# Kernel optimization log

Hardware: AMD Instinct MI355X
Metric: run time of the kernel (lower is better)

The kernel has to match this reference:

```python
import jax, jax.numpy as jnp
import numpy as np

N_NODES = 100000
N_EDGES = 3200000
FEAT = 64  # pos(32) + vel(32)
OUT_DIM = 2


def setup_inputs() -> dict:
    key = jax.random.key(0)
    k1, k2, k3, k4, k5, k6, k7, k8 = jax.random.split(key, 8)
    pos = jax.random.normal(k1, (N_NODES, 32), dtype=jnp.float32)
    vel = jax.random.normal(k2, (N_NODES, 32), dtype=jnp.float32)
    edge_index = jax.random.randint(k3, (2, N_EDGES), 0, N_NODES, dtype=jnp.int64 if jax.config.jax_enable_x64 else jnp.int32)
    s = 1.0 / np.sqrt(FEAT)
    W_rel = jax.random.uniform(k4, (FEAT, FEAT), jnp.float32, -s, s)
    b_rel = jax.random.uniform(k5, (FEAT,), jnp.float32, -s, s)
    W_root = jax.random.uniform(k6, (FEAT, FEAT), jnp.float32, -s, s)
    W_pred = jax.random.uniform(k7, (FEAT, OUT_DIM), jnp.float32, -s, s)
    b_pred = jax.random.uniform(k8, (OUT_DIM,), jnp.float32, -s, s)
    return {"pos": pos, "vel": vel, "edge_index": edge_index,
            "W_rel": W_rel, "b_rel": b_rel, "W_root": W_root,
            "W_pred": W_pred, "b_pred": b_pred}


def reference(pos, vel, edge_index, W_rel, b_rel, W_root, W_pred, b_pred):
    # h = cat([pos, vel], -1)  -> [N, 64]
    h = jnp.concatenate([pos, vel], axis=-1)
    src, dst = edge_index[0], edge_index[1]
    # GraphConv (PyG, aggr='add'): out_i = lin_rel(sum_{j->i} h_j) + lin_root(h_i)
    msgs = h[src]  # [E, 64] irregular gather
    agg = jax.ops.segment_sum(msgs, dst, num_segments=N_NODES)  # [N, 64]
    conv_out = agg @ W_rel + b_rel + h @ W_root
    # lin_pred
    return conv_out @ W_pred + b_pred
```

## Files before the change

### kernel.cpp

```cpp
#include <hip/hip_runtime.h>

#define N_NODES 100000
#define N_EDGES 3200000
#define FEAT 64
#define OUT_DIM 2

#define K_DST 98
#define DST_SZ 1024
#define NPART 8
#define PART_SZ 12500
#define NSUB (K_DST * NPART)
#define CAP_SUB 4468
#define NB 400
#define EPB (N_EDGES / NB)
#define BT 1024


__global__ __launch_bounds__(256) void node_kernel(const float* __restrict__ pos,
                                                   const float* __restrict__ vel,
                                                   const float* __restrict__ W_rel,
                                                   const float* __restrict__ b_rel,
                                                   const float* __restrict__ W_root,
                                                   const float* __restrict__ W_pred,
                                                   const float* __restrict__ b_pred,
                                                   unsigned* __restrict__ y,
                                                   float* __restrict__ out,
                                                   int* __restrict__ gcount) {
    __shared__ float sM[258];
    int t = threadIdx.x;

    if (blockIdx.x == 0)
        for (int i = t; i < NSUB; i += 256) gcount[i] = 0;

    {
        const float* W = (t < 128) ? W_rel : W_root;
        int k = (t & 127) >> 1, o = t & 1;
        float acc = 0.f;
        #pragma unroll
        for (int f = 0; f < FEAT; ++f) acc += W[k * FEAT + f] * W_pred[f * OUT_DIM + o];
        sM[t] = acc;
        if (t < OUT_DIM) {
            float b = b_pred[t];
            #pragma unroll
            for (int f = 0; f < FEAT; ++f) b += b_rel[f] * W_pred[f * OUT_DIM + t];
            sM[256 + t] = b;
        }
    }
    __syncthreads();

    int n = blockIdx.x * 256 + t;
    if (n >= N_NODES) return;

    const float4* p4 = (const float4*)(pos + (size_t)n * 32);
    const float4* v4 = (const float4*)(vel + (size_t)n * 32);
    float h[FEAT];
    #pragma unroll
    for (int i = 0; i < 8; ++i) {
        float4 a = p4[i];
        h[i * 4 + 0] = a.x; h[i * 4 + 1] = a.y; h[i * 4 + 2] = a.z; h[i * 4 + 3] = a.w;
    }
    #pragma unroll
    for (int i = 0; i < 8; ++i) {
        float4 a = v4[i];
        h[32 + i * 4 + 0] = a.x; h[32 + i * 4 + 1] = a.y; h[32 + i * 4 + 2] = a.z; h[32 + i * 4 + 3] = a.w;
    }

    float rel0 = 0.f, rel1 = 0.f, ro0 = 0.f, ro1 = 0.f;
    #pragma unroll
    for (int k = 0; k < FEAT; ++k) {
        float hk = h[k];
        rel0 += hk * sM[2 * k + 0];
        rel1 += hk * sM[2 * k + 1];
        ro0  += hk * sM[128 + 2 * k + 0];
        ro1  += hk * sM[128 + 2 * k + 1];
    }
    unsigned bx = __float_as_uint(rel0);
    unsigned by = __float_as_uint(rel1);
    bx += 0x7FFFu + ((bx >> 16) & 1u);
    by += 0x7FFFu + ((by >> 16) & 1u);
    y[n] = (bx >> 16) | (by & 0xFFFF0000u);
    ((float2*)out)[n] = make_float2(ro0 + sM[256], ro1 + sM[257]);
}

__global__ __launch_bounds__(BT) void binscatter_kernel(const int* __restrict__ edges,
                                                        int* __restrict__ gcount,
                                                        unsigned* __restrict__ scat) {
    __shared__ int hist[NSUB];
    __shared__ int cum[NSUB + 1];
    __shared__ int base[NSUB];
    __shared__ int rpos[NSUB];
    __shared__ unsigned sortbuf[EPB];

    int t = threadIdx.x;
    for (int i = t; i < NSUB; i += BT) hist[i] = 0;
    __syncthreads();

    const int4* s4 = (const int4*)(edges) + blockIdx.x * (EPB / 4);
    const int4* d4 = (const int4*)(edges + N_EDGES) + blockIdx.x * (EPB / 4);
    int4 sreg[2], dreg[2];
    bool valid[2];
    #pragma unroll
    for (int r = 0; r < 2; ++r) {
        int i = t + r * BT;
        valid[r] = (i < EPB / 4);
        if (valid[r]) { sreg[r] = s4[i]; dreg[r] = d4[i]; }
    }

    #pragma unroll
    for (int r = 0; r < 2; ++r) {
        if (!valid[r]) continue;
        int4 s = sreg[r];
        int4 d = dreg[r];
        atomicAdd(&hist[((unsigned)d.x >> 10) * NPART + (unsigned)s.x / PART_SZ], 1);
        atomicAdd(&hist[((unsigned)d.y >> 10) * NPART + (unsigned)s.y / PART_SZ], 1);
        atomicAdd(&hist[((unsigned)d.z >> 10) * NPART + (unsigned)s.z / PART_SZ], 1);
        atomicAdd(&hist[((unsigned)d.w >> 10) * NPART + (unsigned)s.w / PART_SZ], 1);
    }
    __syncthreads();

    for (int i = t; i < NSUB; i += BT) base[i] = atomicAdd(&gcount[i], hist[i]);
    if (t < 64) {
        int lo = t * 13;
        int vals[13];
        int lsum = 0;
        #pragma unroll
        for (int j = 0; j < 13; ++j) {
            int idx = lo + j;
            int v = (idx < NSUB) ? hist[idx] : 0;
            vals[j] = lsum;
            lsum += v;
        }
        int x = lsum;
        #pragma unroll
        for (int d = 1; d < 64; d <<= 1) {
            int up = __shfl_up(x, d);
            if (t >= d) x += up;
        }
        int excl = x - lsum;
        #pragma unroll
        for (int j = 0; j < 13; ++j) {
            int idx = lo + j;
            if (idx < NSUB) { cum[idx] = excl + vals[j]; rpos[idx] = excl + vals[j]; }
        }
        if (t == 63) cum[NSUB] = excl + lsum;
    }
    __syncthreads();

    #pragma unroll
    for (int r = 0; r < 2; ++r) {
        if (!valid[r]) continue;
        int4 s = sreg[r];
        int4 d = dreg[r];
        int k, p;
        k = ((unsigned)d.x >> 10) * NPART + (unsigned)s.x / PART_SZ;
        p = atomicAdd(&rpos[k], 1);
        sortbuf[p] = (unsigned)s.x | (((unsigned)d.x & (DST_SZ - 1)) << 17);
        k = ((unsigned)d.y >> 10) * NPART + (unsigned)s.y / PART_SZ;
        p = atomicAdd(&rpos[k], 1);
        sortbuf[p] = (unsigned)s.y | (((unsigned)d.y & (DST_SZ - 1)) << 17);
        k = ((unsigned)d.z >> 10) * NPART + (unsigned)s.z / PART_SZ;
        p = atomicAdd(&rpos[k], 1);
        sortbuf[p] = (unsigned)s.z | (((unsigned)d.z & (DST_SZ - 1)) << 17);
        k = ((unsigned)d.w >> 10) * NPART + (unsigned)s.w / PART_SZ;
        p = atomicAdd(&rpos[k], 1);
        sortbuf[p] = (unsigned)s.w | (((unsigned)d.w & (DST_SZ - 1)) << 17);
    }
    __syncthreads();

    int wid = t >> 6, lane = t & 63;
    for (int k = wid; k < NSUB; k += BT / 64) {
        int s0 = cum[k], s1 = cum[k + 1], b = base[k];
        for (int j = s0 + lane; j < s1; j += 64) {
            int p = b + (j - s0);
            if (p < CAP_SUB) scat[(size_t)k * CAP_SUB + p] = sortbuf[j];
        }
    }
}

__global__ __launch_bounds__(BT) void accum_partial_kernel(const unsigned* __restrict__ scat,
                                                           const int* __restrict__ gcount,
                                                           const unsigned* __restrict__ y,
                                                           unsigned* __restrict__ partial) {
    __shared__ unsigned yl[PART_SZ];
    __shared__ float accx[DST_SZ];
    __shared__ float accy[DST_SZ];

    int t = threadIdx.x;
    int sub = blockIdx.x;
    int p = sub & (NPART - 1);
    accx[t] = 0.f;
    accy[t] = 0.f;

    const unsigned* yp = y + p * PART_SZ;
    for (int i = t; i < PART_SZ; i += BT) yl[i] = yp[i];
    __syncthreads();

    int c = gcount[sub];
    if (c > CAP_SUB) c = CAP_SUB;
    const unsigned* sl = scat + (size_t)sub * CAP_SUB;
    int pbase = p * PART_SZ;
    for (int i = t; i < c; i += BT) {
        unsigned e = sl[i];
        int slocal = (int)(e & 0x1FFFF) - pbase;
        int dl = e >> 17;
        unsigned v = yl[slocal];
        atomicAdd(&accx[dl], __uint_as_float(v << 16));
        atomicAdd(&accy[dl], __uint_as_float(v & 0xFFFF0000u));
    }
    __syncthreads();

    unsigned bx = __float_as_uint(accx[t]);
    unsigned by = __float_as_uint(accy[t]);
    bx += 0x7FFFu + ((bx >> 16) & 1u);
    by += 0x7FFFu + ((by >> 16) & 1u);
    partial[(size_t)sub * DST_SZ + t] = (bx >> 16) | (by & 0xFFFF0000u);
}

__global__ __launch_bounds__(BT) void merge_kernel(const unsigned* __restrict__ partial,
                                                   float* __restrict__ out) {
    int t = threadIdx.x;
    int kd = blockIdx.x;
    int n = kd * DST_SZ + t;
    if (n >= N_NODES) return;

    float sx = 0.f, sy = 0.f;
    #pragma unroll
    for (int p = 0; p < NPART; ++p) {
        unsigned v = partial[((size_t)kd * NPART + p) * DST_SZ + t];
        sx += __uint_as_float(v << 16);
        sy += __uint_as_float(v & 0xFFFF0000u);
    }
    float2* o2 = (float2*)out;
    float2 cv = o2[n];
    cv.x += sx;
    cv.y += sy;
    o2[n] = cv;
}

extern "C" void kernel_launch(void* const* d_in, const int* in_sizes, int n_in,
                              void* d_out, int out_size, void* d_ws, size_t ws_size,
                              hipStream_t stream) {
    const float* pos    = (const float*)d_in[0];
    const float* vel    = (const float*)d_in[1];
    const int*   edges  = (const int*)d_in[2];
    const float* W_rel  = (const float*)d_in[3];
    const float* b_rel  = (const float*)d_in[4];
    const float* W_root = (const float*)d_in[5];
    const float* W_pred = (const float*)d_in[6];
    const float* b_pred = (const float*)d_in[7];
    float* out = (float*)d_out;

    char* ws = (char*)d_ws;
    unsigned* y       = (unsigned*)(ws + 2048);
    int*      gcount  = (int*)(ws + 402048);
    unsigned* scat    = (unsigned*)(ws + 405184);
    unsigned* partial = (unsigned*)(ws + 14416832);

    int node_blocks = (N_NODES + 255) / 256;
    node_kernel<<<node_blocks, 256, 0, stream>>>(pos, vel, W_rel, b_rel, W_root,
                                                 W_pred, b_pred, y, out, gcount);

    binscatter_kernel<<<NB, BT, 0, stream>>>(edges, gcount, scat);

    accum_partial_kernel<<<NSUB, BT, 0, stream>>>(scat, gcount, y, partial);

    merge_kernel<<<K_DST, BT, 0, stream>>>(partial, out);
}
```

Baseline: 180.8 us.

## Retile destination buckets to 1568 nodes and vectorize partial accumulation loads

The destination bucket size grows from 1024 to 1568 nodes, which cuts the number of sub-buckets from 784 to 512 and raises the per-bucket capacity. The scan is simplified to match. The accumulation kernel now issues all of its global loads up front: node values and edge records are read as uint4 and kept in registers before the shared-memory fill. Each edge chunk is processed in one pass with no loop, and an occupancy hint is added to the launch bounds. This aims to cut block count, per-block overhead and load latency. The cost is a non-power-of-two divide and modulo on destination indices, plus a merge kernel that now computes bucket coordinates per node.

```diff
diff --git a/kernel.cpp b/kernel.cpp
--- a/kernel.cpp
+++ b/kernel.cpp
@@ -5,12 +5,12 @@
 #define FEAT 64
 #define OUT_DIM 2
 
-#define K_DST 98
-#define DST_SZ 1024
+#define K_DST 64
+#define DST_SZ 1568
 #define NPART 8
 #define PART_SZ 12500
 #define NSUB (K_DST * NPART)
-#define CAP_SUB 4468
+#define CAP_SUB 6724
 #define NB 400
 #define EPB (N_EDGES / NB)
 #define BT 1024
@@ -111,25 +111,20 @@
         if (!valid[r]) continue;
         int4 s = sreg[r];
         int4 d = dreg[r];
-        atomicAdd(&hist[((unsigned)d.x >> 10) * NPART + (unsigned)s.x / PART_SZ], 1);
-        atomicAdd(&hist[((unsigned)d.y >> 10) * NPART + (unsigned)s.y / PART_SZ], 1);
-        atomicAdd(&hist[((unsigned)d.z >> 10) * NPART + (unsigned)s.z / PART_SZ], 1);
-        atomicAdd(&hist[((unsigned)d.w >> 10) * NPART + (unsigned)s.w / PART_SZ], 1);
+        atomicAdd(&hist[((unsigned)d.x / DST_SZ) * NPART + (unsigned)s.x / PART_SZ], 1);
+        atomicAdd(&hist[((unsigned)d.y / DST_SZ) * NPART + (unsigned)s.y / PART_SZ], 1);
+        atomicAdd(&hist[((unsigned)d.z / DST_SZ) * NPART + (unsigned)s.z / PART_SZ], 1);
+        atomicAdd(&hist[((unsigned)d.w / DST_SZ) * NPART + (unsigned)s.w / PART_SZ], 1);
     }
     __syncthreads();
 
     for (int i = t; i < NSUB; i += BT) base[i] = atomicAdd(&gcount[i], hist[i]);
     if (t < 64) {
-        int lo = t * 13;
-        int vals[13];
+        int lo = t * 8;
+        int vals[8];
         int lsum = 0;
         #pragma unroll
-        for (int j = 0; j < 13; ++j) {
-            int idx = lo + j;
-            int v = (idx < NSUB) ? hist[idx] : 0;
-            vals[j] = lsum;
-            lsum += v;
-        }
+        for (int j = 0; j < 8; ++j) { int v = hist[lo + j]; vals[j] = lsum; lsum += v; }
         int x = lsum;
         #pragma unroll
         for (int d = 1; d < 64; d <<= 1) {
@@ -138,10 +133,7 @@
         }
         int excl = x - lsum;
         #pragma unroll
-        for (int j = 0; j < 13; ++j) {
-            int idx = lo + j;
-            if (idx < NSUB) { cum[idx] = excl + vals[j]; rpos[idx] = excl + vals[j]; }
-        }
+        for (int j = 0; j < 8; ++j) { cum[lo + j] = excl + vals[j]; rpos[lo + j] = excl + vals[j]; }
         if (t == 63) cum[NSUB] = excl + lsum;
     }
     __syncthreads();
@@ -151,19 +143,19 @@
         if (!valid[r]) continue;
         int4 s = sreg[r];
         int4 d = dreg[r];
-        int k, p;
-        k = ((unsigned)d.x >> 10) * NPART + (unsigned)s.x / PART_SZ;
-        p = atomicAdd(&rpos[k], 1);
-        sortbuf[p] = (unsigned)s.x | (((unsigned)d.x & (DST_SZ - 1)) << 17);
-        k = ((unsigned)d.y >> 10) * NPART + (unsigned)s.y / PART_SZ;
-        p = atomicAdd(&rpos[k], 1);
-        sortbuf[p] = (unsigned)s.y | (((unsigned)d.y & (DST_SZ - 1)) << 17);
-        k = ((unsigned)d.z >> 10) * NPART + (unsigned)s.z / PART_SZ;
-        p = atomicAdd(&rpos[k], 1);
-        sortbuf[p] = (unsigned)s.z | (((unsigned)d.z & (DST_SZ - 1)) << 17);
-        k = ((unsigned)d.w >> 10) * NPART + (unsigned)s.w / PART_SZ;
-        p = atomicAdd(&rpos[k], 1);
-        sortbuf[p] = (unsigned)s.w | (((unsigned)d.w & (DST_SZ - 1)) << 17);
+        int kk, p, dl;
+        kk = (unsigned)d.x / DST_SZ; dl = d.x - kk * DST_SZ;
+        p = atomicAdd(&rpos[kk * NPART + (unsigned)s.x / PART_SZ], 1);
+        sortbuf[p] = (unsigned)s.x | ((unsigned)dl << 17);
+        kk = (unsigned)d.y / DST_SZ; dl = d.y - kk * DST_SZ;
+        p = atomicAdd(&rpos[kk * NPART + (unsigned)s.y / PART_SZ], 1);
+        sortbuf[p] = (unsigned)s.y | ((unsigned)dl << 17);
+        kk = (unsigned)d.z / DST_SZ; dl = d.z - kk * DST_SZ;
+        p = atomicAdd(&rpos[kk * NPART + (unsigned)s.z / PART_SZ], 1);
+        sortbuf[p] = (unsigned)s.z | ((unsigned)dl << 17);
+        kk = (unsigned)d.w / DST_SZ; dl = d.w - kk * DST_SZ;
+        p = atomicAdd(&rpos[kk * NPART + (unsigned)s.w / PART_SZ], 1);
+        sortbuf[p] = (unsigned)s.w | ((unsigned)dl << 17);
     }
     __syncthreads();
 
@@ -177,56 +169,90 @@
     }
 }
 
-__global__ __launch_bounds__(BT) void accum_partial_kernel(const unsigned* __restrict__ scat,
-                                                           const int* __restrict__ gcount,
-                                                           const unsigned* __restrict__ y,
-                                                           unsigned* __restrict__ partial) {
+__global__ __launch_bounds__(BT, 8) void accum_partial_kernel(const unsigned* __restrict__ scat,
+                                                              const int* __restrict__ gcount,
+                                                              const unsigned* __restrict__ y,
+                                                              unsigned* __restrict__ partial) {
     __shared__ unsigned yl[PART_SZ];
     __shared__ float accx[DST_SZ];
     __shared__ float accy[DST_SZ];
 
-    int t = threadIdx.x;
-    int sub = blockIdx.x;
-    int p = sub & (NPART - 1);
-    accx[t] = 0.f;
-    accy[t] = 0.f;
-
-    const unsigned* yp = y + p * PART_SZ;
-    for (int i = t; i < PART_SZ; i += BT) yl[i] = yp[i];
-    __syncthreads();
+    const int t = threadIdx.x;
+    const int sub = blockIdx.x;
+    const int p = sub & (NPART - 1);
 
     int c = gcount[sub];
     if (c > CAP_SUB) c = CAP_SUB;
-    const unsigned* sl = scat + (size_t)sub * CAP_SUB;
-    int pbase = p * PART_SZ;
-    for (int i = t; i < c; i += BT) {
-        unsigned e = sl[i];
-        int slocal = (int)(e & 0x1FFFF) - pbase;
-        int dl = e >> 17;
-        unsigned v = yl[slocal];
-        atomicAdd(&accx[dl], __uint_as_float(v << 16));
-        atomicAdd(&accy[dl], __uint_as_float(v & 0xFFFF0000u));
-    }
-    __syncthreads();
-
-    unsigned bx = __float_as_uint(accx[t]);
-    unsigned by = __float_as_uint(accy[t]);
-    bx += 0x7FFFu + ((bx >> 16) & 1u);
-    by += 0x7FFFu + ((by >> 16) & 1u);
-    partial[(size_t)sub * DST_SZ + t] = (bx >> 16) | (by & 0xFFFF0000u);
+    const int nq = (c + 3) >> 2;
+
+    const uint4* y4 = (const uint4*)(y) + p * (PART_SZ / 4);
+    uint4 q0 = y4[t];
+    uint4 q1 = y4[t + BT];
+    uint4 q2 = y4[t + 2 * BT];
+    uint4 q3;
+    const bool s3 = t < (PART_SZ / 4 - 3 * BT);
+    if (s3) q3 = y4[t + 3 * BT];
+
+    const uint4* sc4 = (const uint4*)(scat + (size_t)sub * CAP_SUB);
+    uint4 e0, e1;
+    const bool g0 = t < nq, g1 = (t + BT) < nq;
+    if (g0) e0 = sc4[t];
+    if (g1) e1 = sc4[t + BT];
+
+    for (int i = t; i < DST_SZ; i += BT) { accx[i] = 0.f; accy[i] = 0.f; }
+
+    uint4* yl4 = (uint4*)yl;
+    yl4[t] = q0;
+    yl4[t + BT] = q1;
+    yl4[t + 2 * BT] = q2;
+    if (s3) yl4[t + 3 * BT] = q3;
+    __syncthreads();
+
+    const int pbase = p * PART_SZ;
+    if (g0) {
+        int eidx = t << 2;
+        unsigned v0 = yl[(int)(e0.x & 0x1FFFF) - pbase];
+        unsigned v1 = yl[(int)(e0.y & 0x1FFFF) - pbase];
+        unsigned v2 = yl[(int)(e0.z & 0x1FFFF) - pbase];
+        unsigned v3 = yl[(int)(e0.w & 0x1FFFF) - pbase];
+        if (eidx + 0 < c) { atomicAdd(&accx[e0.x >> 17], __uint_as_float(v0 << 16)); atomicAdd(&accy[e0.x >> 17], __uint_as_float(v0 & 0xFFFF0000u)); }
+        if (eidx + 1 < c) { atomicAdd(&accx[e0.y >> 17], __uint_as_float(v1 << 16)); atomicAdd(&accy[e0.y >> 17], __uint_as_float(v1 & 0xFFFF0000u)); }
+        if (eidx + 2 < c) { atomicAdd(&accx[e0.z >> 17], __uint_as_float(v2 << 16)); atomicAdd(&accy[e0.z >> 17], __uint_as_float(v2 & 0xFFFF0000u)); }
+        if (eidx + 3 < c) { atomicAdd(&accx[e0.w >> 17], __uint_as_float(v3 << 16)); atomicAdd(&accy[e0.w >> 17], __uint_as_float(v3 & 0xFFFF0000u)); }
+    }
+    if (g1) {
+        int eidx = (t + BT) << 2;
+        unsigned v0 = yl[(int)(e1.x & 0x1FFFF) - pbase];
+        unsigned v1 = yl[(int)(e1.y & 0x1FFFF) - pbase];
+        unsigned v2 = yl[(int)(e1.z & 0x1FFFF) - pbase];
+        unsigned v3 = yl[(int)(e1.w & 0x1FFFF) - pbase];
+        if (eidx + 0 < c) { atomicAdd(&accx[e1.x >> 17], __uint_as_float(v0 << 16)); atomicAdd(&accy[e1.x >> 17], __uint_as_float(v0 & 0xFFFF0000u)); }
+        if (eidx + 1 < c) { atomicAdd(&accx[e1.y >> 17], __uint_as_float(v1 << 16)); atomicAdd(&accy[e1.y >> 17], __uint_as_float(v1 & 0xFFFF0000u)); }
+        if (eidx + 2 < c) { atomicAdd(&accx[e1.z >> 17], __uint_as_float(v2 << 16)); atomicAdd(&accy[e1.z >> 17], __uint_as_float(v2 & 0xFFFF0000u)); }
+        if (eidx + 3 < c) { atomicAdd(&accx[e1.w >> 17], __uint_as_float(v3 << 16)); atomicAdd(&accy[e1.w >> 17], __uint_as_float(v3 & 0xFFFF0000u)); }
+    }
+    __syncthreads();
+
+    for (int i = t; i < DST_SZ; i += BT) {
+        unsigned bx = __float_as_uint(accx[i]);
+        unsigned by = __float_as_uint(accy[i]);
+        bx += 0x7FFFu + ((bx >> 16) & 1u);
+        by += 0x7FFFu + ((by >> 16) & 1u);
+        partial[(size_t)sub * DST_SZ + i] = (bx >> 16) | (by & 0xFFFF0000u);
+    }
 }
 
 __global__ __launch_bounds__(BT) void merge_kernel(const unsigned* __restrict__ partial,
                                                    float* __restrict__ out) {
-    int t = threadIdx.x;
-    int kd = blockIdx.x;
-    int n = kd * DST_SZ + t;
+    int n = blockIdx.x * BT + threadIdx.x;
     if (n >= N_NODES) return;
+    unsigned kd = (unsigned)n / DST_SZ;
+    int dl = n - kd * DST_SZ;
 
     float sx = 0.f, sy = 0.f;
     #pragma unroll
     for (int p = 0; p < NPART; ++p) {
-        unsigned v = partial[((size_t)kd * NPART + p) * DST_SZ + t];
+        unsigned v = partial[((size_t)(kd * NPART + p)) * DST_SZ + dl];
         sx += __uint_as_float(v << 16);
         sy += __uint_as_float(v & 0xFFFF0000u);
     }
@@ -253,8 +279,8 @@
     char* ws = (char*)d_ws;
     unsigned* y       = (unsigned*)(ws + 2048);
     int*      gcount  = (int*)(ws + 402048);
-    unsigned* scat    = (unsigned*)(ws + 405184);
-    unsigned* partial = (unsigned*)(ws + 14416832);
+    unsigned* scat    = (unsigned*)(ws + 404096);
+    unsigned* partial = (unsigned*)(ws + 14174848);
 
     int node_blocks = (N_NODES + 255) / 256;
     node_kernel<<<node_blocks, 256, 0, stream>>>(pos, vel, W_rel, b_rel, W_root,
@@ -264,5 +290,5 @@
 
     accum_partial_kernel<<<NSUB, BT, 0, stream>>>(scat, gcount, y, partial);
 
-    merge_kernel<<<K_DST, BT, 0, stream>>>(partial, out);
-}
+    merge_kernel<<<98, BT, 0, stream>>>(partial, out);
+}
```

Result: faster. 162.3 us (-10.3%).
